# Kernel tuning notes

Measured on AMD Instinct MI355X. Metric: run time of the kernel, lower is better.

## Reference

```python
import jax, jax.numpy as jnp
import numpy as np

D_MODEL = 1024
D_STATE = 16
D_CONV = 4
EXPAND = 2
D_INNER = EXPAND * D_MODEL          # 2048
DT_RANK = (D_MODEL + 15) // 16      # 64
BSZ, T0, H0, W0 = 4, 8, 16, 16
SEQLEN = T0 * H0 * W0               # 2048
N_BANDS = 8


def setup_inputs() -> dict:
    key = jax.random.key(0)
    ks = jax.random.split(key, 8)
    hidden_states = jax.random.normal(ks[0], (BSZ, SEQLEN, D_MODEL), jnp.float32)
    in_proj_w = jax.random.normal(ks[1], (2 * D_INNER, D_MODEL), jnp.float32) * (D_MODEL ** -0.5)
    conv_w = jax.random.normal(ks[2], (D_INNER, 1, D_CONV), jnp.float32) * (D_CONV ** -0.5)
    conv_b = jnp.zeros((D_INNER,), jnp.float32)
    x_proj_w = jax.random.normal(ks[3], (DT_RANK + 2 * D_STATE, D_INNER), jnp.float32) * (D_INNER ** -0.5)
    dt_std = DT_RANK ** -0.5
    dt_proj_w = jax.random.uniform(ks[4], (D_INNER, DT_RANK), jnp.float32, -dt_std, dt_std)
    # inverse-softplus init of dt bias, as in the torch module
    dt = jnp.exp(jax.random.uniform(ks[5], (D_INNER,), jnp.float32)
                 * (np.log(0.1) - np.log(0.001)) + np.log(0.001))
    dt = jnp.clip(dt, 1e-4, None)
    dt_proj_b = dt + jnp.log(-jnp.expm1(-dt))
    A_log = jnp.log(jnp.tile(jnp.arange(1, D_STATE + 1, dtype=jnp.float32)[None, :], (D_INNER, 1)))
    D_param = jnp.ones((D_INNER,), jnp.float32)
    out_proj_w = jax.random.normal(ks[6], (D_MODEL, D_INNER), jnp.float32) * (D_INNER ** -0.5)
    return dict(hidden_states=hidden_states, T=T0, H=H0, W=W0,
                in_proj_w=in_proj_w, conv_w=conv_w, conv_b=conv_b,
                x_proj_w=x_proj_w, dt_proj_w=dt_proj_w, dt_proj_b=dt_proj_b,
                A_log=A_log, D=D_param, out_proj_w=out_proj_w)


def _channel_alignment(x, B, T, H, W):
    """x: (B, C, L=T*H*W) -> (align_loss scalar, features (B*T, C))."""
    C = x.shape[1]
    x4 = x.reshape(B, C, T, H, W).transpose(0, 2, 1, 3, 4).reshape(B * T, C, H, W)
    fr = jnp.fft.rfft2(x4, axes=(-2, -1))
    mag = jnp.sqrt(fr.real ** 2 + fr.imag ** 2 + 1e-8)
    mag = jnp.fft.fftshift(mag, axes=(-2, -1))
    Wr = mag.shape[-1]                      # W//2 + 1
    hg = jnp.arange(H)[:, None]
    wg = jnp.arange(Wr)[None, :]
    r = jnp.sqrt(((hg - H // 2) / H) ** 2 + ((wg - Wr // 2) / Wr) ** 2)
    masks = jnp.stack([((r >= i / N_BANDS) & (r < (i + 1) / N_BANDS)).astype(mag.dtype)
                       for i in range(N_BANDS)])          # (8, H, Wr)
    bands = jnp.einsum('bchw,khw->bck', mag, masks)        # (B*T, C, 8)
    bands = bands / (bands.sum(-1, keepdims=True) + 1e-8)
    features = bands[..., N_BANDS // 2:].sum(-1)           # (B*T, C) high-freq ratio
    fn = features / jnp.maximum(jnp.linalg.norm(features, axis=1, keepdims=True), 1e-12)
    sim = fn @ fn.T
    Bt = features.shape[0]
    loss = 1.0 - sim.sum() / (Bt * Bt)
    return loss, features


def _invert_A(A_log, features):
    """Blend A_log toward its column-flipped version, weighted by channel features."""
    A_max = A_log.max(axis=0, keepdims=True)
    A_min = A_log.min(axis=0, keepdims=True)
    A_flipped = A_max + A_min - A_log
    attention = jnp.linalg.norm(jnp.exp(A_log), axis=1)
    attention = attention / (attention.max() + 1e-8)
    f = jax.nn.softmax(jax.lax.stop_gradient(features).mean(axis=0))
    alpha = jnp.clip(f * (1.0 - attention), 0.0, 1.0)[:, None]   # (d_inner, 1)
    return (1.0 - alpha) * A_log + alpha * A_flipped


def reference(hidden_states, T, H, W, in_proj_w, conv_w, conv_b,
              x_proj_w, dt_proj_w, dt_proj_b, A_log, D, out_proj_w):
    B, L, _ = hidden_states.shape
    xz = jnp.einsum('bld,ed->bel', hidden_states, in_proj_w)      # (B, 2*d_inner, L)
    x, z = xz[:, :D_INNER], xz[:, D_INNER:]

    align_loss, features = _channel_alignment(x, B, T, H, W)
    A_log_new = _invert_A(A_log, features)
    A = -jnp.exp(A_log_new)                                       # (d_inner, d_state)

    # causal depthwise conv1d + SiLU (left pad d_conv-1 == torch pad then slice :L)
    xc = jax.lax.conv_general_dilated(x, conv_w, (1,), [(D_CONV - 1, 0)],
                                      dimension_numbers=('NCH', 'OIH', 'NCH'),
                                      feature_group_count=D_INNER)
    xc = jax.nn.silu(xc + conv_b[None, :, None])                  # (B, d_inner, L)

    x_dbl = jnp.einsum('bdl,ed->ble', xc, x_proj_w)               # (B, L, dt_rank+2N)
    dt_low = x_dbl[..., :DT_RANK]
    Bm = x_dbl[..., DT_RANK:DT_RANK + D_STATE]                    # (B, L, N)
    Cm = x_dbl[..., DT_RANK + D_STATE:]                           # (B, L, N)
    delta = jax.nn.softplus(jnp.einsum('blr,dr->bld', dt_low, dt_proj_w) + dt_proj_b)

    u = xc.transpose(0, 2, 1)                                     # (B, L, d_inner)

    def step(s, inp):
        d_t, u_t, B_t, C_t = inp                                  # (B,D),(B,D),(B,N),(B,N)
        s = s * jnp.exp(d_t[..., None] * A) + (d_t * u_t)[..., None] * B_t[:, None, :]
        y_t = jnp.einsum('bdn,bn->bd', s, C_t)
        return s, y_t

    s0 = jnp.zeros((B, D_INNER, D_STATE), delta.dtype)
    _, ys = jax.lax.scan(step, s0,
                         (delta.transpose(1, 0, 2), u.transpose(1, 0, 2),
                          Bm.transpose(1, 0, 2), Cm.transpose(1, 0, 2)))
    y = ys.transpose(1, 0, 2)                                     # (B, L, d_inner)
    y = y + u * D
    y = y * jax.nn.silu(z.transpose(0, 2, 1))
    out = jnp.einsum('bld,ed->ble', y, out_proj_w)                # (B, L, d_model)
    return out, align_loss
```

## Files before the change

kernel.cpp:

```cpp
#include <hip/hip_runtime.h>
#include <math.h>
#include <stdint.h>

#define LSEQ 2048
#define DM   1024
#define DI   2048
#define NC   32
#define CL   64

#define OFF_X     ((size_t)0)
#define OFF_Z     ((size_t)16777216)
#define OFF_U     ((size_t)33554432)
#define OFF_S     ((size_t)50331648)
#define OFF_CS    (OFF_S)
#define OFF_SDT   (OFF_S + 4194304)
#define OFF_XDBL  (OFF_S + 4456448)
#define OFF_FEAT  (OFF_S + 5242880)
#define OFF_AWS   (OFF_S + 5308448)
#define OFF_B1    ((size_t)58720256)

__device__ __forceinline__ float silu_(float x) { return x / (1.f + __expf(-x)); }
__device__ __forceinline__ float softplus_(float x) {
  return fmaxf(x, 0.f) + log1pf(__expf(-fabsf(x)));
}
__device__ __forceinline__ unsigned short f2bf(float x) {
  unsigned int u = __float_as_uint(x);
  u += 0x7fffu + ((u >> 16) & 1u);
  return (unsigned short)(u >> 16);
}
__device__ __forceinline__ float bf2f(unsigned short h) {
  return __uint_as_float(((unsigned int)h) << 16);
}

typedef __attribute__((ext_vector_type(8))) short bf16x8;
typedef __attribute__((ext_vector_type(4))) float f32x4;

__device__ __forceinline__ void gl2lds16(const void* g, void* l) {
  __builtin_amdgcn_global_load_lds(
      (const __attribute__((address_space(1))) unsigned int*)(uintptr_t)g,
      (__attribute__((address_space(3))) unsigned int*)(uintptr_t)l,
      16, 0, 0);
}

__global__ __launch_bounds__(256) void split2_w(
    const float* __restrict__ a, unsigned short* __restrict__ oa, int ksa,
    size_t na4,
    const float* __restrict__ b, unsigned short* __restrict__ ob, int ksb)
{
  size_t i4 = ((size_t)blockIdx.x << 8) + threadIdx.x;
  const float* src; unsigned short* dst; int ks;
  if (i4 < na4) { src = a; dst = oa; ks = ksa; }
  else          { src = b; dst = ob; ks = ksb; i4 -= na4; }
  const size_t flat = i4 << 2;
  const int K = 1 << ks;
  const size_t row = flat >> ks;
  const int k = (int)(flat & (size_t)(K - 1));
  float4 v = *(const float4*)(src + flat);
  float f[4] = {v.x, v.y, v.z, v.w};
  unsigned short h[4], lo[4];
#pragma unroll
  for (int c = 0; c < 4; ++c) { h[c] = f2bf(f[c]); lo[c] = f2bf(f[c] - bf2f(h[c])); }
  unsigned short* o = dst + (row << (ks + 1)) + k;
  *(uint2*)(o)     = make_uint2((unsigned)h[0]  | ((unsigned)h[1]  << 16),
                                (unsigned)h[2]  | ((unsigned)h[3]  << 16));
  *(uint2*)(o + K) = make_uint2((unsigned)lo[0] | ((unsigned)lo[1] << 16),
                                (unsigned)lo[2] | ((unsigned)lo[3] << 16));
}

template <int NPASS, int A_FP32>
__global__ __launch_bounds__(256) void gemm_mfma(
    const void* __restrict__ Avp, const unsigned short* __restrict__ Bp,
    float* __restrict__ C, int K, int ldc, int nxs)
{
  __shared__ unsigned short AsH[128 * 32];
  __shared__ unsigned short BsH[128 * 32];
  __shared__ unsigned short AsL[(NPASS > 1) ? 128 * 32 : 8];
  __shared__ unsigned short BsL[(NPASS > 1) ? 128 * 32 : 8];
  const int tid = threadIdx.x;
  const int lin = blockIdx.y * gridDim.x + blockIdx.x;
  const int xcd = lin & 7;
  const int t = lin >> 3;
  const int nmask = (1 << nxs) - 1;
  const int bn = (((t & nmask) << 3) | xcd) << 7;
  const int bm = (t >> nxs) << 7;
  const int K2 = K * 2;

  const int wave = tid >> 6, lane = tid & 63;
  const int wm = (wave >> 1) << 6, wn = (wave & 1) << 6;
  const int lm = lane & 15, quad = lane >> 4;
  const int sw = (lm >> 1) & 3;

  f32x4 acc[4][4] = {};

  const int r0 = tid >> 2;
  const int kq = ((tid & 3) ^ ((r0 >> 1) & 3)) << 3;
  const unsigned short* BgH0 = Bp + (size_t)(bn + r0) * K2 + kq;
  const unsigned short* BgH1 = Bp + (size_t)(bn + 64 + r0) * K2 + kq;
  unsigned short* lA0 = &AsH[(size_t)tid * 8];
  unsigned short* lA1 = &AsH[(size_t)(256 + tid) * 8];
  unsigned short* lB0 = &BsH[(size_t)tid * 8];
  unsigned short* lB1 = &BsH[(size_t)(256 + tid) * 8];
  unsigned short* lAl0 = (NPASS > 1) ? &AsL[(size_t)tid * 8] : nullptr;
  unsigned short* lAl1 = (NPASS > 1) ? &AsL[(size_t)(256 + tid) * 8] : nullptr;
  unsigned short* lBl0 = (NPASS > 1) ? &BsL[(size_t)tid * 8] : nullptr;
  unsigned short* lBl1 = (NPASS > 1) ? &BsL[(size_t)(256 + tid) * 8] : nullptr;

  const unsigned short* AgH0 = nullptr; const unsigned short* AgH1 = nullptr;
  const float* Af0 = nullptr; const float* Af1 = nullptr;
  if (A_FP32) {
    const float* Af = (const float*)Avp;
    Af0 = Af + (size_t)(bm + r0) * K + kq;
    Af1 = Af + (size_t)(bm + 64 + r0) * K + kq;
  } else {
    const unsigned short* Ab = (const unsigned short*)Avp;
    AgH0 = Ab + (size_t)(bm + r0) * K2 + kq;
    AgH1 = Ab + (size_t)(bm + 64 + r0) * K2 + kq;
  }

  for (int k0 = 0; k0 < K; k0 += 32) {
    __syncthreads();
    if (A_FP32) {
      float4 u0 = *(const float4*)(Af0 + k0);
      float4 u1 = *(const float4*)(Af0 + k0 + 4);
      float4 v0 = *(const float4*)(Af1 + k0);
      float4 v1 = *(const float4*)(Af1 + k0 + 4);
      float fu[8] = {u0.x,u0.y,u0.z,u0.w,u1.x,u1.y,u1.z,u1.w};
      float fv[8] = {v0.x,v0.y,v0.z,v0.w,v1.x,v1.y,v1.z,v1.w};
      unsigned int hu[4], lu[4], hv[4], lv[4];
#pragma unroll
      for (int c = 0; c < 4; ++c) {
        unsigned short h0 = f2bf(fu[2*c]),   l0 = f2bf(fu[2*c]   - bf2f(h0));
        unsigned short h1 = f2bf(fu[2*c+1]), l1 = f2bf(fu[2*c+1] - bf2f(h1));
        hu[c] = (unsigned)h0 | ((unsigned)h1 << 16);
        lu[c] = (unsigned)l0 | ((unsigned)l1 << 16);
        unsigned short g0 = f2bf(fv[2*c]),   m0 = f2bf(fv[2*c]   - bf2f(g0));
        unsigned short g1 = f2bf(fv[2*c+1]), m1 = f2bf(fv[2*c+1] - bf2f(g1));
        hv[c] = (unsigned)g0 | ((unsigned)g1 << 16);
        lv[c] = (unsigned)m0 | ((unsigned)m1 << 16);
      }
      *(uint4*)lA0  = make_uint4(hu[0], hu[1], hu[2], hu[3]);
      *(uint4*)lA1  = make_uint4(hv[0], hv[1], hv[2], hv[3]);
      if (NPASS > 1) {
        *(uint4*)lAl0 = make_uint4(lu[0], lu[1], lu[2], lu[3]);
        *(uint4*)lAl1 = make_uint4(lv[0], lv[1], lv[2], lv[3]);
      }
    } else {
      gl2lds16(AgH0 + k0, lA0);
      gl2lds16(AgH1 + k0, lA1);
      if (NPASS > 1) {
        gl2lds16(AgH0 + K + k0, lAl0);
        gl2lds16(AgH1 + K + k0, lAl1);
      }
    }
    gl2lds16(BgH0 + k0, lB0);
    gl2lds16(BgH1 + k0, lB1);
    if (NPASS > 1) {
      gl2lds16(BgH0 + K + k0, lBl0);
      gl2lds16(BgH1 + K + k0, lBl1);
    }
    __syncthreads();

    bf16x8 aH[4], bH[4];
#pragma unroll
    for (int i = 0; i < 4; ++i)
      aH[i] = *(const bf16x8*)&AsH[(wm + i * 16 + lm) * 32 + ((quad ^ sw) << 3)];
#pragma unroll
    for (int j = 0; j < 4; ++j)
      bH[j] = *(const bf16x8*)&BsH[(wn + j * 16 + lm) * 32 + ((quad ^ sw) << 3)];
#pragma unroll
    for (int i = 0; i < 4; ++i)
#pragma unroll
      for (int j = 0; j < 4; ++j)
        acc[i][j] = __builtin_amdgcn_mfma_f32_16x16x32_bf16(aH[i], bH[j], acc[i][j], 0, 0, 0);
    if (NPASS > 1) {
      bf16x8 aL[4], bL[4];
#pragma unroll
      for (int i = 0; i < 4; ++i)
        aL[i] = *(const bf16x8*)&AsL[(wm + i * 16 + lm) * 32 + ((quad ^ sw) << 3)];
#pragma unroll
      for (int j = 0; j < 4; ++j)
        bL[j] = *(const bf16x8*)&BsL[(wn + j * 16 + lm) * 32 + ((quad ^ sw) << 3)];
#pragma unroll
      for (int i = 0; i < 4; ++i)
#pragma unroll
        for (int j = 0; j < 4; ++j) {
          acc[i][j] = __builtin_amdgcn_mfma_f32_16x16x32_bf16(aH[i], bL[j], acc[i][j], 0, 0, 0);
          acc[i][j] = __builtin_amdgcn_mfma_f32_16x16x32_bf16(aL[i], bH[j], acc[i][j], 0, 0, 0);
        }
    }
  }

#pragma unroll
  for (int i = 0; i < 4; ++i) {
    const int m = bm + wm + i * 16 + quad * 4;
#pragma unroll
    for (int j = 0; j < 4; ++j) {
      const int n = bn + wn + j * 16 + lm;
#pragma unroll
      for (int r = 0; r < 4; ++r)
        C[(size_t)(m + r) * ldc + n] = acc[i][j][r];
    }
  }
}

template <int EPI>
__global__ __launch_bounds__(256) void gemm_nt(
    const float* __restrict__ A, int lda,
    const float* __restrict__ B, int ldb,
    float* __restrict__ C, int ldc,
    int N, int K, const float* __restrict__ bias, size_t cseg)
{
  __shared__ float As[16][68];
  __shared__ float Bs[16][68];
  const int tid = threadIdx.x;
  const int bm = blockIdx.y << 6;
  const int bn = blockIdx.x << 6;
  const int kz = blockIdx.z;
  A += (size_t)kz * K;
  B += (size_t)kz * K;
  C += (size_t)kz * cseg;
  const int lr = tid >> 2;
  const int lk = (tid & 3) << 2;
  const int tx = tid & 15, ty = tid >> 4;

  float acc[4][4];
#pragma unroll
  for (int i = 0; i < 4; ++i)
#pragma unroll
    for (int j = 0; j < 4; ++j) acc[i][j] = 0.f;

  const float* Apt = A + (size_t)(bm + lr) * lda + lk;
  const float* Bpt = B + (size_t)(bn + lr) * ldb + lk;
  const bool bv = (bn + lr) < N;

  for (int k0 = 0; k0 < K; k0 += 16) {
    float4 a4 = *(const float4*)(Apt + k0);
    float4 b4 = bv ? *(const float4*)(Bpt + k0) : make_float4(0.f, 0.f, 0.f, 0.f);
    __syncthreads();
    As[lk + 0][lr] = a4.x; As[lk + 1][lr] = a4.y;
    As[lk + 2][lr] = a4.z; As[lk + 3][lr] = a4.w;
    Bs[lk + 0][lr] = b4.x; Bs[lk + 1][lr] = b4.y;
    Bs[lk + 2][lr] = b4.z; Bs[lk + 3][lr] = b4.w;
    __syncthreads();
#pragma unroll
    for (int k = 0; k < 16; ++k) {
      const float4 av = *(const float4*)(&As[k][ty << 2]);
      const float4 bw = *(const float4*)(&Bs[k][tx << 2]);
      float a4r[4] = {av.x, av.y, av.z, av.w};
      float b4r[4] = {bw.x, bw.y, bw.z, bw.w};
#pragma unroll
      for (int i = 0; i < 4; ++i)
#pragma unroll
        for (int j = 0; j < 4; ++j)
          acc[i][j] = fmaf(a4r[i], b4r[j], acc[i][j]);
    }
  }

  const int m = bm + (ty << 2);
  const int n = bn + (tx << 2);
#pragma unroll
  for (int i = 0; i < 4; ++i) {
    float v[4] = {acc[i][0], acc[i][1], acc[i][2], acc[i][3]};
    if (EPI == 1) {
#pragma unroll
      for (int j = 0; j < 4; ++j)
        if (n + j < N) v[j] = softplus_(v[j] + bias[n + j]);
    }
    if (n + 3 < N) {
      *(float4*)(C + (size_t)(m + i) * ldc + n) = make_float4(v[0], v[1], v[2], v[3]);
    } else {
#pragma unroll
      for (int j = 0; j < 4; ++j)
        if (n + j < N) C[(size_t)(m + i) * ldc + n + j] = v[j];
    }
  }
}

__global__ __launch_bounds__(256) void reduce4(
    const float* __restrict__ P, float* __restrict__ O, size_t seg)
{
  const size_t i = ((size_t)blockIdx.x << 8) + threadIdx.x;
  float4 a = ((const float4*)P)[i];
  float4 b = ((const float4*)(P + seg))[i];
  float4 c = ((const float4*)(P + 2 * seg))[i];
  float4 d = ((const float4*)(P + 3 * seg))[i];
  ((float4*)O)[i] = make_float4(a.x + b.x + c.x + d.x,
                                a.y + b.y + c.y + d.y,
                                a.z + b.z + c.z + d.z,
                                a.w + b.w + c.w + d.w);
}

__global__ __launch_bounds__(256) void feat_kernel(
    const float* __restrict__ X, float* __restrict__ features)
{
  __shared__ float xin[256][17];
  __shared__ float Rf[16 * 315];
  __shared__ float tc[16], ts[16];
  __shared__ float part2[16][16][2];

  const int tid = threadIdx.x;
  const int frame = blockIdx.x >> 7;
  const int cg = blockIdx.x & 127;
  const int b = frame >> 3, t = frame & 7;
  const int c0 = cg << 4;

  if (tid < 16) {
    float ang = 0.39269908169872414f * (float)tid;
    tc[tid] = cosf(ang);
    ts[tid] = sinf(ang);
  }
  const float* xb = X + ((size_t)(b * LSEQ + t * 256) << 11) + c0;
  for (int i = tid; i < 256 * 16; i += 256) {
    int hw = i >> 4, ci = i & 15;
    xin[hw][ci] = xb[((size_t)hw << 11) + ci];
  }
  __syncthreads();

  {
    const int ci = tid & 15, h = tid >> 4;
    float re[9], im[9];
#pragma unroll
    for (int kw = 0; kw < 9; ++kw) { re[kw] = 0.f; im[kw] = 0.f; }
#pragma unroll
    for (int w = 0; w < 16; ++w) {
      float x = xin[(h << 4) + w][ci];
#pragma unroll
      for (int kw = 0; kw < 9; ++kw) {
        int ph = (kw * w) & 15;
        re[kw] = fmaf(x, tc[ph], re[kw]);
        im[kw] = fmaf(-x, ts[ph], im[kw]);
      }
    }
#pragma unroll
    for (int kw = 0; kw < 9; ++kw) {
      Rf[ci * 315 + kw * 35 + 2 * h]     = re[kw];
      Rf[ci * 315 + kw * 35 + 2 * h + 1] = im[kw];
    }
  }
  __syncthreads();

  {
    const int ci = tid & 15, kh = tid >> 4;
    float ut = 0.f, tt = 0.f;
    for (int kw = 0; kw < 9; ++kw) {
      float fre = 0.f, fim = 0.f;
#pragma unroll
      for (int h = 0; h < 16; ++h) {
        int ph = (kh * h) & 15;
        float c = tc[ph], s = ts[ph];
        float rr = Rf[ci * 315 + kw * 35 + 2 * h];
        float ri = Rf[ci * 315 + kw * 35 + 2 * h + 1];
        fre += rr * c + ri * s;
        fim += ri * c - rr * s;
      }
      float mag = sqrtf(fre * fre + fim * fim + 1e-8f);
      int sh = (kh + 8) & 15;
      int sw2 = kw + 4; if (sw2 >= 9) sw2 -= 9;
      float dh = (float)(sh - 8) / 16.0f;
      float dw = (float)(sw2 - 4) / 9.0f;
      tt += mag;
      if (dh * dh + dw * dw >= 0.25f) ut += mag;
    }
    part2[ci][kh][0] = ut;
    part2[ci][kh][1] = tt;
  }
  __syncthreads();

  if (tid < 16) {
    float ut = 0.f, tt = 0.f;
    for (int kh = 0; kh < 16; ++kh) { ut += part2[tid][kh][0]; tt += part2[tid][kh][1]; }
    features[frame * DI + c0 + tid] = ut / (tt + 1e-8f);
  }
}

__global__ __launch_bounds__(256) void alpha_kernel(
    const float* __restrict__ feats, const float* __restrict__ A_log,
    float* __restrict__ Aws, float* __restrict__ loss_out)
{
  __shared__ float red[256];
  __shared__ float invn[32];
  __shared__ float PT[32][257];
  __shared__ float AM[256][17];
  __shared__ float sAmax[16], sAmin[16];
  const int tid = threadIdx.x;

  float pn[32];
#pragma unroll
  for (int i = 0; i < 32; ++i) pn[i] = 0.f;
  float md[8];
#pragma unroll
  for (int j = 0; j < 8; ++j) md[j] = 0.f;
  for (int i = 0; i < 32; ++i) {
#pragma unroll
    for (int j = 0; j < 8; ++j) {
      float v = feats[(i << 11) + tid + (j << 8)];
      pn[i] = fmaf(v, v, pn[i]);
      md[j] += v;
    }
  }
#pragma unroll
  for (int j = 0; j < 8; ++j) md[j] *= (1.f / 32.f);
#pragma unroll
  for (int i = 0; i < 32; ++i) PT[i][tid] = pn[i];
  __syncthreads();
  if (tid < 32) {
    float s = 0.f;
    for (int k = 0; k < 256; ++k) s += PT[tid][k];
    invn[tid] = 1.f / fmaxf(sqrtf(s), 1e-12f);
  }
  __syncthreads();

  float gsq = 0.f;
#pragma unroll
  for (int j = 0; j < 8; ++j) {
    float gd = 0.f;
    for (int i = 0; i < 32; ++i)
      gd = fmaf(feats[(i << 11) + tid + (j << 8)], invn[i], gd);
    gsq = fmaf(gd, gd, gsq);
  }
  red[tid] = gsq; __syncthreads();
  for (int s = 128; s > 0; s >>= 1) { if (tid < s) red[tid] += red[tid + s]; __syncthreads(); }
  if (tid == 0) loss_out[0] = 1.f - red[0] * (1.f / 1024.f);
  __syncthreads();

  float lm = md[0];
#pragma unroll
  for (int j = 1; j < 8; ++j) lm = fmaxf(lm, md[j]);
  red[tid] = lm; __syncthreads();
  for (int s = 128; s > 0; s >>= 1) { if (tid < s) red[tid] = fmaxf(red[tid], red[tid + s]); __syncthreads(); }
  const float mmax = red[0]; __syncthreads();

  float p[8]; float ps = 0.f;
#pragma unroll
  for (int j = 0; j < 8; ++j) { p[j] = __expf(md[j] - mmax); ps += p[j]; }
  red[tid] = ps; __syncthreads();
  for (int s = 128; s > 0; s >>= 1) { if (tid < s) red[tid] += red[tid + s]; __syncthreads(); }
  const float psum = red[0]; __syncthreads();

  float amaxl[16], aminl[16], rn[8];
#pragma unroll
  for (int n = 0; n < 16; ++n) { amaxl[n] = -1e30f; aminl[n] = 1e30f; }
#pragma unroll
  for (int j = 0; j < 8; ++j) {
    const int d = tid + (j << 8);
    float ss = 0.f;
#pragma unroll
    for (int n = 0; n < 16; ++n) {
      float a = A_log[(d << 4) + n];
      float e = __expf(a);
      ss = fmaf(e, e, ss);
      amaxl[n] = fmaxf(amaxl[n], a);
      aminl[n] = fminf(aminl[n], a);
    }
    rn[j] = sqrtf(ss);
  }
  float rm = rn[0];
#pragma unroll
  for (int j = 1; j < 8; ++j) rm = fmaxf(rm, rn[j]);
  red[tid] = rm; __syncthreads();
  for (int s = 128; s > 0; s >>= 1) { if (tid < s) red[tid] = fmaxf(red[tid], red[tid + s]); __syncthreads(); }
  const float rnmax = red[0]; __syncthreads();

#pragma unroll
  for (int n = 0; n < 16; ++n) AM[tid][n] = amaxl[n];
  __syncthreads();
  if (tid < 16) { float m = -1e30f; for (int i = 0; i < 256; ++i) m = fmaxf(m, AM[i][tid]); sAmax[tid] = m; }
  __syncthreads();
#pragma unroll
  for (int n = 0; n < 16; ++n) AM[tid][n] = aminl[n];
  __syncthreads();
  if (tid < 16) { float m = 1e30f; for (int i = 0; i < 256; ++i) m = fminf(m, AM[i][tid]); sAmin[tid] = m; }
  __syncthreads();

  const float irn = 1.f / (rnmax + 1e-8f);
#pragma unroll
  for (int j = 0; j < 8; ++j) {
    const int d = tid + (j << 8);
    const float att = rn[j] * irn;
    const float f = p[j] / psum;
    const float alpha = fminf(fmaxf(f * (1.f - att), 0.f), 1.f);
#pragma unroll
    for (int n = 0; n < 16; ++n) {
      float a = A_log[(d << 4) + n];
      float fl = sAmax[n] + sAmin[n] - a;
      float an = (1.f - alpha) * a + alpha * fl;
      Aws[(d << 4) + n] = -__expf(an);
    }
  }
}

__global__ __launch_bounds__(256) void conv_kernel(
    const float* __restrict__ X, const float* __restrict__ cw,
    const float* __restrict__ cb, float* __restrict__ U)
{
  const size_t i4 = ((size_t)blockIdx.x << 8) + threadIdx.x;
  const int e4 = (int)(i4 & 511);
  const size_t row = i4 >> 9;
  const int l = (int)(row & 2047);
  const float* xr = X + (row << 11) + (e4 << 2);
  const float4 z4 = make_float4(0.f, 0.f, 0.f, 0.f);
  float4 x0 = *(const float4*)xr;
  float4 x1 = (l >= 1) ? *(const float4*)(xr - 2048) : z4;
  float4 x2 = (l >= 2) ? *(const float4*)(xr - 4096) : z4;
  float4 x3 = (l >= 3) ? *(const float4*)(xr - 6144) : z4;
  const float4* cwf = (const float4*)cw;
  float4 bi = *(const float4*)(cb + (e4 << 2));
  float x0a[4] = {x0.x, x0.y, x0.z, x0.w};
  float x1a[4] = {x1.x, x1.y, x1.z, x1.w};
  float x2a[4] = {x2.x, x2.y, x2.z, x2.w};
  float x3a[4] = {x3.x, x3.y, x3.z, x3.w};
  float bia[4] = {bi.x, bi.y, bi.z, bi.w};
  float o[4];
#pragma unroll
  for (int c = 0; c < 4; ++c) {
    float4 w = cwf[(e4 << 2) + c];
    float acc = bia[c];
    acc = fmaf(x3a[c], w.x, acc);
    acc = fmaf(x2a[c], w.y, acc);
    acc = fmaf(x1a[c], w.z, acc);
    acc = fmaf(x0a[c], w.w, acc);
    o[c] = silu_(acc);
  }
  *(float4*)(U + (i4 << 2)) = make_float4(o[0], o[1], o[2], o[3]);
}

__global__ __launch_bounds__(256) void scan_pass1(
    const float* __restrict__ delta, const float* __restrict__ U,
    const float* __restrict__ xdbl, const float* __restrict__ Aws,
    float* __restrict__ cs, float* __restrict__ sdt)
{
  __shared__ float blds[CL * 16];
  const int tid = threadIdx.x;
  const int dg = blockIdx.x & 7;
  const int chunk = (blockIdx.x >> 3) & 31;
  const int b = blockIdx.x >> 8;
  const int d = (dg << 8) | tid;
  const int l0 = chunk * CL;

  for (int i = tid; i < CL * 16; i += 256) {
    int l = i >> 4, j = i & 15;
    blds[i] = xdbl[(size_t)(b * LSEQ + l0 + l) * 96 + 64 + j];
  }
  __syncthreads();

  float Ar[16];
#pragma unroll
  for (int n = 0; n < 16; ++n) Ar[n] = Aws[(d << 4) + n];
  float s[16];
#pragma unroll
  for (int n = 0; n < 16; ++n) s[n] = 0.f;
  float sumdt = 0.f;

  const float* dp = delta + ((size_t)b << 22) + ((size_t)l0 << 11) + d;
  const float* up = U + ((size_t)b << 22) + ((size_t)l0 << 11) + d;

  for (int l = 0; l < CL; ++l) {
    const float dt = dp[(size_t)l << 11];
    const float u = up[(size_t)l << 11];
    sumdt += dt;
    const float du = dt * u;
    const float* bl = &blds[l << 4];
#pragma unroll
    for (int n = 0; n < 16; ++n)
      s[n] = fmaf(s[n], __expf(dt * Ar[n]), du * bl[n]);
  }

  float* csp = cs + ((((size_t)b * NC + chunk) * 2048 + d) << 4);
#pragma unroll
  for (int n = 0; n < 4; ++n)
    *(float4*)(csp + (n << 2)) = make_float4(s[4*n], s[4*n+1], s[4*n+2], s[4*n+3]);
  sdt[((size_t)b * NC + chunk) * 2048 + d] = sumdt;
}

__global__ __launch_bounds__(256) void scan_mid(
    float* __restrict__ cs, const float* __restrict__ sdt,
    const float* __restrict__ Aws)
{
  const int b = blockIdx.x >> 3;
  const int d = ((blockIdx.x & 7) << 8) | threadIdx.x;
  float Ar[16];
#pragma unroll
  for (int n = 0; n < 16; ++n) Ar[n] = Aws[(d << 4) + n];
  float si[16];
#pragma unroll
  for (int n = 0; n < 16; ++n) si[n] = 0.f;

  for (int c = 0; c < NC; ++c) {
    const size_t base = ((size_t)b * NC + c) * 2048 + d;
    float* csp = cs + (base << 4);
    float sl[16];
#pragma unroll
    for (int n = 0; n < 4; ++n) {
      float4 v = *(const float4*)(csp + (n << 2));
      sl[4*n] = v.x; sl[4*n+1] = v.y; sl[4*n+2] = v.z; sl[4*n+3] = v.w;
    }
    const float sm = sdt[base];
#pragma unroll
    for (int n = 0; n < 4; ++n)
      *(float4*)(csp + (n << 2)) = make_float4(si[4*n], si[4*n+1], si[4*n+2], si[4*n+3]);
#pragma unroll
    for (int n = 0; n < 16; ++n)
      si[n] = fmaf(si[n], __expf(sm * Ar[n]), sl[n]);
  }
}

__global__ __launch_bounds__(256) void scan_pass3(
    const float* __restrict__ delta, const float* __restrict__ Z,
    float* __restrict__ U,
    const float* __restrict__ xdbl, const float* __restrict__ Aws,
    const float* __restrict__ Dp, const float* __restrict__ cs)
{
  __shared__ float bclds[CL * 32];
  const int tid = threadIdx.x;
  const int dg = blockIdx.x & 7;
  const int chunk = (blockIdx.x >> 3) & 31;
  const int b = blockIdx.x >> 8;
  const int d = (dg << 8) | tid;
  const int l0 = chunk * CL;

  for (int i = tid; i < CL * 32; i += 256) {
    int l = i >> 5, j = i & 31;
    bclds[i] = xdbl[(size_t)(b * LSEQ + l0 + l) * 96 + 64 + j];
  }
  __syncthreads();

  float Ar[16];
#pragma unroll
  for (int n = 0; n < 16; ++n) Ar[n] = Aws[(d << 4) + n];
  const float Dd = Dp[d];

  const float* csp = cs + ((((size_t)b * NC + chunk) * 2048 + d) << 4);
  float s[16];
#pragma unroll
  for (int n = 0; n < 4; ++n) {
    float4 v = *(const float4*)(csp + (n << 2));
    s[4*n] = v.x; s[4*n+1] = v.y; s[4*n+2] = v.z; s[4*n+3] = v.w;
  }

  const float* dp = delta + ((size_t)b << 22) + ((size_t)l0 << 11) + d;
  const float* zp = Z + ((size_t)b << 22) + ((size_t)l0 << 11) + d;
  float* up = U + ((size_t)b << 22) + ((size_t)l0 << 11) + d;

  for (int l = 0; l < CL; ++l) {
    const float dt = dp[(size_t)l << 11];
    const float u = up[(size_t)l << 11];
    const float z = zp[(size_t)l << 11];
    const float du = dt * u;
    const float* bcl = &bclds[l << 5];
    float y = 0.f;
#pragma unroll
    for (int n = 0; n < 16; ++n) {
      s[n] = fmaf(s[n], __expf(dt * Ar[n]), du * bcl[n]);
      y = fmaf(s[n], bcl[16 + n], y);
    }
    const float yv = fmaf(u, Dd, y);
    up[(size_t)l << 11] = yv * silu_(z);
  }
}

extern "C" void kernel_launch(void* const* d_in, const int* in_sizes, int n_in,
                              void* d_out, int out_size, void* d_ws, size_t ws_size,
                              hipStream_t stream)
{
  const float* hs         = (const float*)d_in[0];
  const float* in_proj_w  = (const float*)d_in[4];
  const float* conv_w     = (const float*)d_in[5];
  const float* conv_b     = (const float*)d_in[6];
  const float* x_proj_w   = (const float*)d_in[7];
  const float* dt_proj_w  = (const float*)d_in[8];
  const float* dt_proj_b  = (const float*)d_in[9];
  const float* A_log      = (const float*)d_in[10];
  const float* Dp         = (const float*)d_in[11];
  const float* out_proj_w = (const float*)d_in[12];
  float* out = (float*)d_out;
  float* ws = (float*)d_ws;

  float* X     = ws + OFF_X;
  float* Z     = ws + OFF_Z;
  float* U     = ws + OFF_U;
  float* cs    = ws + OFF_CS;
  float* sdt   = ws + OFF_SDT;
  float* xdbl  = ws + OFF_XDBL;
  float* feats = ws + OFF_FEAT;
  float* Aws   = ws + OFF_AWS;
  unsigned short* A1s = (unsigned short*)(ws + OFF_S);
  unsigned short* B1s = (unsigned short*)(ws + OFF_B1);
  unsigned short* B2s = (unsigned short*)(ws + OFF_B1);

  const dim3 blk(256);

  split2_w<<<12288, blk, 0, stream>>>(hs, A1s, 10, (size_t)2097152,
                                      in_proj_w, B1s, 10);
  gemm_mfma<3, 0><<<dim3(16, 64), blk, 0, stream>>>(A1s, B1s, X, 1024, 2048, 1);
  gemm_mfma<1, 0><<<dim3(16, 64), blk, 0, stream>>>(A1s, B1s + (size_t)2048 * 2048, Z, 1024, 2048, 1);
  feat_kernel<<<4096, blk, 0, stream>>>(X, feats);
  conv_kernel<<<16384, blk, 0, stream>>>(X, conv_w, conv_b, U);
  split2_w<<<2048, blk, 0, stream>>>(out_proj_w, B2s, 11, (size_t)524288,
                                     out_proj_w, B2s, 11);
  alpha_kernel<<<1, blk, 0, stream>>>(feats, A_log, Aws, out + 8388608);
  gemm_nt<0><<<dim3(2, 128, 4), blk, 0, stream>>>(U, DI, x_proj_w, DI, cs, 96, 96, 512, nullptr, (size_t)786432);
  reduce4<<<768, blk, 0, stream>>>(cs, xdbl, (size_t)786432);
  gemm_nt<1><<<dim3(32, 128, 1), blk, 0, stream>>>(xdbl, 96, dt_proj_w, 64, X, DI, DI, 64, dt_proj_b, 0);
  scan_pass1<<<1024, blk, 0, stream>>>(X, U, xdbl, Aws, cs, sdt);
  scan_mid<<<32, blk, 0, stream>>>(cs, sdt, Aws);
  scan_pass3<<<1024, blk, 0, stream>>>(X, Z, U, xdbl, Aws, Dp, cs);
  gemm_mfma<3, 1><<<dim3(8, 64), blk, 0, stream>>>(U, B2s, out, 2048, 1024, 0);
}
```

Baseline: 944.1 us.

## Add 256x256 double-buffered phased MFMA GEMM for in_proj and use exp2 in scans

Replaces the 128x128 in_proj GEMMs with a 512-thread 256x256-tile kernel. It double-buffers LDS via direct global-to-LDS loads and splits each k-step into four MFMA phases, interleaving loads with compute and raising wave priority. Separately, the A matrix is pre-scaled by log2(e) so the scan kernels can use hardware exp2 instead of expf. The larger tile raises data reuse but uses a lot of LDS, which limits occupancy, and adds many barriers.

```diff
diff --git a/kernel.cpp b/kernel.cpp
--- a/kernel.cpp
+++ b/kernel.cpp
@@ -41,6 +41,13 @@
       (__attribute__((address_space(3))) unsigned int*)(uintptr_t)l,
       16, 0, 0);
 }
+
+#define BARRIER_()                                   \
+  do {                                               \
+    asm volatile("" ::: "memory");                   \
+    __builtin_amdgcn_s_barrier();                    \
+    asm volatile("" ::: "memory");                   \
+  } while (0)
 
 __global__ __launch_bounds__(256) void split2_w(
     const float* __restrict__ a, unsigned short* __restrict__ oa, int ksa,
@@ -65,6 +72,140 @@
                                 (unsigned)h[2]  | ((unsigned)h[3]  << 16));
   *(uint2*)(o + K) = make_uint2((unsigned)lo[0] | ((unsigned)lo[1] << 16),
                                 (unsigned)lo[2] | ((unsigned)lo[3] << 16));
+}
+
+template <int NPASS, int MH, int NH>
+__device__ __forceinline__ void phase_mfma(
+    const unsigned short* __restrict__ shc, f32x4 (&acc)[8][4],
+    int wm, int wn, int lm, int roff)
+{
+  bf16x8 aH[4], bH[2], aL[4], bL[2];
+#pragma unroll
+  for (int ii = 0; ii < 4; ++ii) {
+    const int ar = (wm + (MH * 4 + ii) * 16 + lm) * 32 + roff;
+    aH[ii] = *(const bf16x8*)(shc + ar);
+    if constexpr (NPASS > 1) aL[ii] = *(const bf16x8*)(shc + 2 * 8192 + ar);
+  }
+#pragma unroll
+  for (int jj = 0; jj < 2; ++jj) {
+    const int br = (wn + (NH * 2 + jj) * 16 + lm) * 32 + roff;
+    bH[jj] = *(const bf16x8*)(shc + 8192 + br);
+    if constexpr (NPASS > 1) bL[jj] = *(const bf16x8*)(shc + 3 * 8192 + br);
+  }
+  __builtin_amdgcn_s_setprio(1);
+#pragma unroll
+  for (int ii = 0; ii < 4; ++ii)
+#pragma unroll
+    for (int jj = 0; jj < 2; ++jj) {
+      const int i = MH * 4 + ii, j = NH * 2 + jj;
+      acc[i][j] = __builtin_amdgcn_mfma_f32_16x16x32_bf16(aH[ii], bH[jj], acc[i][j], 0, 0, 0);
+      if constexpr (NPASS > 1) {
+        acc[i][j] = __builtin_amdgcn_mfma_f32_16x16x32_bf16(aH[ii], bL[jj], acc[i][j], 0, 0, 0);
+        acc[i][j] = __builtin_amdgcn_mfma_f32_16x16x32_bf16(aL[ii], bH[jj], acc[i][j], 0, 0, 0);
+      }
+    }
+  __builtin_amdgcn_s_setprio(0);
+}
+
+template <int NPASS>
+__global__ __launch_bounds__(512, 2) void gemm_8ph(
+    const unsigned short* __restrict__ Ap, const unsigned short* __restrict__ Bp,
+    float* __restrict__ C, int K, int ldc)
+{
+  constexpr int NTEN = (NPASS > 1) ? 4 : 2;
+  __shared__ unsigned short sh[2][NTEN][256 * 32];
+  const int tid = threadIdx.x;
+  const int bn = blockIdx.x << 8;
+  const int bm = blockIdx.y << 8;
+  const int K2 = K * 2;
+  const int wave = tid >> 6, lane = tid & 63;
+  const int wm = (wave >> 2) << 7;
+  const int wn = (wave & 3) << 6;
+  const int lm = lane & 15, quad = lane >> 4;
+  const int roff = ((quad ^ ((lm >> 1) & 3)) << 3);
+
+  const int r0 = tid >> 2;
+  const int kq = (((tid & 3) ^ ((r0 >> 1) & 3)) << 3);
+  const unsigned short* a0 = Ap + (size_t)(bm + r0) * K2 + kq;
+  const unsigned short* a1 = a0 + (size_t)128 * K2;
+  const unsigned short* b0 = Bp + (size_t)(bn + r0) * K2 + kq;
+  const unsigned short* b1 = b0 + (size_t)128 * K2;
+  const int ls0 = tid * 8, ls1 = 4096 + tid * 8;
+
+  f32x4 acc[8][4] = {};
+  const int NT = K >> 5;
+
+  {
+    unsigned short* s = &sh[0][0][0];
+    gl2lds16(a0, s + ls0);
+    gl2lds16(a1, s + ls1);
+    if constexpr (NPASS > 1) {
+      gl2lds16(a0 + K, s + 2 * 8192 + ls0);
+      gl2lds16(a1 + K, s + 2 * 8192 + ls1);
+    }
+    gl2lds16(b0, s + 8192 + ls0);
+    gl2lds16(b1, s + 8192 + ls1);
+    if constexpr (NPASS > 1) {
+      gl2lds16(b0 + K, s + 3 * 8192 + ls0);
+      gl2lds16(b1 + K, s + 3 * 8192 + ls1);
+    }
+  }
+
+  for (int t = 0; t < NT - 1; ++t) {
+    const unsigned short* cur = &sh[t & 1][0][0];
+    unsigned short* nxt = &sh[(t + 1) & 1][0][0];
+    const int kn = (t + 1) << 5;
+
+    gl2lds16(a0 + kn, nxt + ls0);
+    gl2lds16(a1 + kn, nxt + ls1);
+    if constexpr (NPASS > 1) {
+      gl2lds16(a0 + K + kn, nxt + 2 * 8192 + ls0);
+      gl2lds16(a1 + K + kn, nxt + 2 * 8192 + ls1);
+      asm volatile("s_waitcnt vmcnt(4)" ::: "memory");
+    } else {
+      asm volatile("s_waitcnt vmcnt(2)" ::: "memory");
+    }
+    BARRIER_();
+    phase_mfma<NPASS, 0, 0>(cur, acc, wm, wn, lm, roff);
+    BARRIER_();
+    gl2lds16(b0 + kn, nxt + 8192 + ls0);
+    gl2lds16(b1 + kn, nxt + 8192 + ls1);
+    if constexpr (NPASS > 1) {
+      gl2lds16(b0 + K + kn, nxt + 3 * 8192 + ls0);
+      gl2lds16(b1 + K + kn, nxt + 3 * 8192 + ls1);
+    }
+    phase_mfma<NPASS, 0, 1>(cur, acc, wm, wn, lm, roff);
+    BARRIER_();
+    phase_mfma<NPASS, 1, 0>(cur, acc, wm, wn, lm, roff);
+    BARRIER_();
+    phase_mfma<NPASS, 1, 1>(cur, acc, wm, wn, lm, roff);
+    BARRIER_();
+  }
+
+  {
+    const unsigned short* cur = &sh[(NT - 1) & 1][0][0];
+    asm volatile("s_waitcnt vmcnt(0)" ::: "memory");
+    BARRIER_();
+    phase_mfma<NPASS, 0, 0>(cur, acc, wm, wn, lm, roff);
+    BARRIER_();
+    phase_mfma<NPASS, 0, 1>(cur, acc, wm, wn, lm, roff);
+    BARRIER_();
+    phase_mfma<NPASS, 1, 0>(cur, acc, wm, wn, lm, roff);
+    BARRIER_();
+    phase_mfma<NPASS, 1, 1>(cur, acc, wm, wn, lm, roff);
+  }
+
+#pragma unroll
+  for (int i = 0; i < 8; ++i) {
+    const int m = bm + wm + i * 16 + quad * 4;
+#pragma unroll
+    for (int j = 0; j < 4; ++j) {
+      const int n = bn + wn + j * 16 + lm;
+#pragma unroll
+      for (int r = 0; r < 4; ++r)
+        C[(size_t)(m + r) * ldc + n] = acc[i][j][r];
+    }
+  }
 }
 
 template <int NPASS, int A_FP32>
@@ -484,7 +625,7 @@
       float a = A_log[(d << 4) + n];
       float fl = sAmax[n] + sAmin[n] - a;
       float an = (1.f - alpha) * a + alpha * fl;
-      Aws[(d << 4) + n] = -__expf(an);
+      Aws[(d << 4) + n] = -__expf(an) * 1.4426950408889634f;
     }
   }
 }
@@ -562,7 +703,7 @@
     const float* bl = &blds[l << 4];
 #pragma unroll
     for (int n = 0; n < 16; ++n)
-      s[n] = fmaf(s[n], __expf(dt * Ar[n]), du * bl[n]);
+      s[n] = fmaf(s[n], __builtin_amdgcn_exp2f(dt * Ar[n]), du * bl[n]);
   }
 
   float* csp = cs + ((((size_t)b * NC + chunk) * 2048 + d) << 4);
@@ -600,7 +741,7 @@
       *(float4*)(csp + (n << 2)) = make_float4(si[4*n], si[4*n+1], si[4*n+2], si[4*n+3]);
 #pragma unroll
     for (int n = 0; n < 16; ++n)
-      si[n] = fmaf(si[n], __expf(sm * Ar[n]), sl[n]);
+      si[n] = fmaf(si[n], __builtin_amdgcn_exp2f(sm * Ar[n]), sl[n]);
   }
 }
 
@@ -650,7 +791,7 @@
     float y = 0.f;
 #pragma unroll
     for (int n = 0; n < 16; ++n) {
-      s[n] = fmaf(s[n], __expf(dt * Ar[n]), du * bcl[n]);
+      s[n] = fmaf(s[n], __builtin_amdgcn_exp2f(dt * Ar[n]), du * bcl[n]);
       y = fmaf(s[n], bcl[16 + n], y);
     }
     const float yv = fmaf(u, Dd, y);
@@ -691,8 +832,8 @@
 
   split2_w<<<12288, blk, 0, stream>>>(hs, A1s, 10, (size_t)2097152,
                                       in_proj_w, B1s, 10);
-  gemm_mfma<3, 0><<<dim3(16, 64), blk, 0, stream>>>(A1s, B1s, X, 1024, 2048, 1);
-  gemm_mfma<1, 0><<<dim3(16, 64), blk, 0, stream>>>(A1s, B1s + (size_t)2048 * 2048, Z, 1024, 2048, 1);
+  gemm_8ph<3><<<dim3(8, 32), dim3(512), 0, stream>>>(A1s, B1s, X, 1024, 2048);
+  gemm_8ph<1><<<dim3(8, 32), dim3(512), 0, stream>>>(A1s, B1s + (size_t)2048 * 2048, Z, 1024, 2048);
   feat_kernel<<<4096, blk, 0, stream>>>(X, feats);
   conv_kernel<<<16384, blk, 0, stream>>>(X, conv_w, conv_b, U);
   split2_w<<<2048, blk, 0, stream>>>(out_proj_w, B2s, 11, (size_t)524288,
```

Result: faster. 883.3 us (-6.4%).
